# Performance work log

Measured on AMD Instinct MI355X. Metric: run time of the kernel, lower is better.

The kernel has to match this reference:

```python
import jax, jax.numpy as jnp
import numpy as np

B, F, H, W = 1, 6, 20, 26
S = F * H * W            # 3120 tokens
DIM, NH, HD = 1536, 12, 128
C = HD // 2              # 64 rotary channels
T_C = C - 2 * (C // 3)   # 22 temporal channels
H_C = C // 3             # 21
W_C = C // 3             # 21
LOCAL_FRAMES = 4         # local_attn_size (in frames)
SINK_FRAMES = 1          # sink_size (in frames)
EPS = 1e-6
MAX_POS = 1024


def _angle_table(n_ch):
    inv = 1.0 / (10000.0 ** (np.arange(n_ch, dtype=np.float64) / n_ch))
    return np.outer(np.arange(MAX_POS, dtype=np.float64), inv)


def setup_inputs() -> dict:
    key = jax.random.key(0)
    ks = jax.random.split(key, 8)
    sc = 0.02
    ang = np.concatenate([_angle_table(T_C), _angle_table(H_C), _angle_table(W_C)], axis=1)  # [1024, 64]
    return {
        "x": jax.random.normal(ks[0], (B, S, DIM), jnp.float32),
        "seq_lens": jnp.array([S], jnp.int32),
        "grid_sizes": jnp.array([[F, H, W]], jnp.int32),
        "freqs_cos": jnp.asarray(np.cos(ang), jnp.float32),
        "freqs_sin": jnp.asarray(np.sin(ang), jnp.float32),
        "Wq": jax.random.normal(ks[1], (DIM, DIM), jnp.float32) * sc,
        "bq": jnp.zeros((DIM,), jnp.float32),
        "Wk": jax.random.normal(ks[2], (DIM, DIM), jnp.float32) * sc,
        "bk": jnp.zeros((DIM,), jnp.float32),
        "Wv": jax.random.normal(ks[3], (DIM, DIM), jnp.float32) * sc,
        "bv": jnp.zeros((DIM,), jnp.float32),
        "Wo": jax.random.normal(ks[4], (DIM, DIM), jnp.float32) * sc,
        "bo": jnp.zeros((DIM,), jnp.float32),
        "gq": jnp.ones((DIM,), jnp.float32),
        "gk": jnp.ones((DIM,), jnp.float32),
    }


def _rms_norm(x, g):
    # WanRMSNorm: x * rsqrt(mean(x^2) + eps) * weight
    return x * jax.lax.rsqrt(jnp.mean(x * x, axis=-1, keepdims=True) + EPS) * g


def _rope_apply(x, freqs_cos, freqs_sin):
    # x: [B, S, NH, HD]; per-token 3D (f,h,w) rotary on consecutive pairs.
    pos = jnp.arange(S)
    f = pos // (H * W)
    hh = (pos // W) % H
    ww = pos % W
    cos_t, cos_h, cos_w = freqs_cos[:, :T_C], freqs_cos[:, T_C:T_C + H_C], freqs_cos[:, T_C + H_C:]
    sin_t, sin_h, sin_w = freqs_sin[:, :T_C], freqs_sin[:, T_C:T_C + H_C], freqs_sin[:, T_C + H_C:]
    cos = jnp.concatenate([cos_t[f], cos_h[hh], cos_w[ww]], axis=-1)[None, :, None, :]  # [1,S,1,C]
    sin = jnp.concatenate([sin_t[f], sin_h[hh], sin_w[ww]], axis=-1)[None, :, None, :]
    xp = x.reshape(B, S, NH, C, 2)
    xr, xi = xp[..., 0], xp[..., 1]
    out = jnp.stack([xr * cos - xi * sin, xr * sin + xi * cos], axis=-1)
    return out.reshape(B, S, NH, HD)


def _block_mask():
    # frame-causal + local window (in frames) + sink frames: [S, S] bool
    fid = jnp.arange(S) // (H * W)
    fi, fj = fid[:, None], fid[None, :]
    return (fj <= fi) & ((fi - fj < LOCAL_FRAMES) | (fj < SINK_FRAMES))


def reference(x, seq_lens, grid_sizes, freqs_cos, freqs_sin,
              Wq, bq, Wk, bk, Wv, bv, Wo, bo, gq, gk):
    q = _rms_norm(x @ Wq + bq, gq).reshape(B, S, NH, HD)
    k = _rms_norm(x @ Wk + bk, gk).reshape(B, S, NH, HD)
    v = (x @ Wv + bv).reshape(B, S, NH, HD)
    rq = _rope_apply(q, freqs_cos, freqs_sin)
    rk = _rope_apply(k, freqs_cos, freqs_sin)
    scale = 1.0 / jnp.sqrt(jnp.asarray(HD, x.dtype))
    scores = jnp.einsum('bind,bjnd->bnij', rq, rk) * scale  # [B,NH,S,S]
    scores = jnp.where(_block_mask()[None, None], scores, jnp.finfo(scores.dtype).min)
    attn = jax.nn.softmax(scores, axis=-1)
    out = jnp.einsum('bnij,bjnd->bind', attn, v).reshape(B, S, DIM)
    return out @ Wo + bo
```

## Files before the change

kernel.cpp:

```cpp
#include <hip/hip_runtime.h>
#include <hip/hip_bf16.h>
#include <stdint.h>

typedef short v8s __attribute__((ext_vector_type(8)));
typedef short v4h __attribute__((ext_vector_type(4)));
typedef float v4f __attribute__((ext_vector_type(4)));
typedef unsigned short u16;

#define S_LEN 3120
#define DIMN 1536
#define NHEAD 12
#define HDIM 128
#define FRM 520
#define NT64 49
#define T64_PH 166
#define TOT64 1992
#define NSTEP32 17
#define SCALE_QK 0.088388347648318447f
#define MAXOFF 12.0f

struct TaskMap {
  unsigned char tile[T64_PH];
  unsigned char frame[T64_PH];
  short accv[NT64];
  unsigned char nf[NT64];
};
constexpr TaskMap make_map() {
  TaskMap m{};
  int acc = 0;
  for (int tile = 0; tile < NT64; ++tile) {
    int q0t = tile * 64;
    int f_lo = q0t / FRM;
    int qhi = q0t + 63 < S_LEN - 1 ? q0t + 63 : S_LEN - 1;
    int f_hi = qhi / FRM;
    int fstart = f_lo - 3 > 0 ? f_lo - 3 : 0;
    int sink = fstart > 0 ? 1 : 0;
    int nf = f_hi - fstart + 1 + sink;
    m.accv[tile] = (short)acc;
    m.nf[tile] = (unsigned char)nf;
    for (int c = 0; c < nf; ++c) {
      m.tile[acc + c] = (unsigned char)tile;
      m.frame[acc + c] = (unsigned char)(sink ? (c == 0 ? 0 : fstart + c - 1) : (fstart + c));
    }
    acc += nf;
  }
  return m;
}
__device__ __constant__ TaskMap TM = make_map();

__device__ __forceinline__ v4f mfma16(v8s a, v8s b, v4f c) {
  return __builtin_amdgcn_mfma_f32_16x16x32_bf16(a, b, c, 0, 0, 0);
}
__device__ __forceinline__ float b2f(u16 u) {
  union { float f; unsigned int i; } x; x.i = ((unsigned int)u) << 16; return x.f;
}
__device__ __forceinline__ u16 f2b(float f) {
  union { float f; unsigned int i; } x; x.f = f;
  unsigned int r = x.i + 0x7FFFu + ((x.i >> 16) & 1u);
  return (u16)(r >> 16);
}
__device__ __forceinline__ void async16(const void* g, void* l) {
  __builtin_amdgcn_global_load_lds(
      (__attribute__((address_space(1))) const void*)g,
      (__attribute__((address_space(3))) void*)l, 16, 0, 0);
}

__global__ void detect_dtype(const u16* __restrict__ w, int* __restrict__ flag) {
  __shared__ int sh;
  int t = threadIdx.x;
  if (t == 0) sh = 0;
  __syncthreads();
  u16 m0 = (u16)(w[2 * t] & 0x7FFF);
  u16 m1 = (u16)(w[2 * t + 1] & 0x7FFF);
  if (m0 >= 0x4480 || m1 >= 0x4480) atomicOr(&sh, 1);
  __syncthreads();
  if (t == 0) *flag = sh;
}

struct PrepArgs {
  const void* tin[4]; u16* tout[4];
  const void* csrc[9]; u16* cdst[9]; int cn[9];
};
__global__ __launch_bounds__(256) void prep(PrepArgs a, const int* __restrict__ flag) {
  int isf = *flag;
  int z = blockIdx.z;
  int t = threadIdx.x;
  int bidx = blockIdx.y * gridDim.x + blockIdx.x;
  if (z < 4) {
    const float* inf = (const float*)a.tin[z];
    const u16* inb = (const u16*)a.tin[z];
    u16* out = a.tout[z];
    int row = (bidx % 24) * 64 + (t & 63);
    int c0 = (bidx / 24) * 16 + (t >> 6) * 4;
    float v[4];
    if (isf) {
      float4 d = *(const float4*)(inf + (size_t)row * DIMN + c0);
      v[0] = d.x; v[1] = d.y; v[2] = d.z; v[3] = d.w;
    } else {
      ushort4 d = *(const ushort4*)(inb + (size_t)row * DIMN + c0);
      v[0] = b2f(d.x); v[1] = b2f(d.y); v[2] = b2f(d.z); v[3] = b2f(d.w);
    }
#pragma unroll
    for (int k = 0; k < 4; ++k)
      out[(size_t)(c0 + k) * DIMN + row] = f2b(v[k]);
  } else {
    int id = z - 4;
    int n4 = a.cn[id] >> 2;
    const float* sf = (const float*)a.csrc[id];
    const u16* sb = (const u16*)a.csrc[id];
    u16* d = a.cdst[id];
    int stride = gridDim.x * gridDim.y * 256;
    for (int i = bidx * 256 + t; i < n4; i += stride) {
      v4h o;
      if (isf) {
        float4 x4 = *(const float4*)(sf + (size_t)i * 4);
        o[0] = (short)f2b(x4.x); o[1] = (short)f2b(x4.y);
        o[2] = (short)f2b(x4.z); o[3] = (short)f2b(x4.w);
      } else {
        o = *(const v4h*)(sb + (size_t)i * 4);
      }
      *(v4h*)(d + (size_t)i * 4) = o;
    }
  }
}

template <int MT, int NT>
__global__ __launch_bounds__(256) void gemm3(
    const u16* __restrict__ A,
    const u16* BT0, const u16* BT1, const u16* BT2,
    const u16* b0, const u16* b1, const u16* b2,
    void* C0, void* C1, void* C2, int M, const int* __restrict__ flag, int dyn) {
  static_assert(MT == 64, "4-wave layout assumes MT==64");
  const u16* BT; const u16* bias; void* C;
  if (blockIdx.z == 0)      { BT = BT0; bias = b0; C = C0; }
  else if (blockIdx.z == 1) { BT = BT1; bias = b1; C = C1; }
  else                      { BT = BT2; bias = b2; C = C2; }
  int f32out = dyn ? *flag : 0;
  __shared__ __align__(16) short As[MT * 64];
  __shared__ __align__(16) short Bs[NT * 64];
  int t = threadIdx.x, w = t >> 6, l = t & 63;
  int ln = l & 15, lg = l >> 4;
  int m0 = blockIdx.y * MT, n0 = blockIdx.x * NT;
  int lr = l >> 3;
  int gl = (l & 7) ^ lr;
  constexpr int ACH = MT / 32;
  constexpr int BCH = NT / 32;
  const u16* gAp[ACH]; short* lAp[ACH];
#pragma unroll
  for (int i = 0; i < ACH; ++i) {
    int c = w * ACH + i;
    int arow = min(m0 + c * 8 + lr, M - 1);
    gAp[i] = A + (size_t)arow * DIMN + gl * 8;
    lAp[i] = As + c * 512;
  }
  const u16* gBp[BCH]; short* lBp[BCH];
#pragma unroll
  for (int i = 0; i < BCH; ++i) {
    int c = w * BCH + i;
    int brow = n0 + c * 8 + lr;
    gBp[i] = BT + (size_t)brow * DIMN + gl * 8;
    lBp[i] = Bs + c * 512;
  }
  constexpr int NJ = NT / 64;
  int aoff[2][4], boff[2][NJ];
#pragma unroll
  for (int ks = 0; ks < 2; ++ks) {
#pragma unroll
    for (int i = 0; i < 4; ++i) {
      int ar = i * 16 + ln;
      aoff[ks][i] = ar * 64 + (((ks * 4 + lg) ^ (ar & 7)) * 8);
    }
#pragma unroll
    for (int j = 0; j < NJ; ++j) {
      int br = w * (NJ * 16) + j * 16 + ln;
      boff[ks][j] = br * 64 + (((ks * 4 + lg) ^ (br & 7)) * 8);
    }
  }
  v4f acc[4][NJ] = {};
  for (int k0 = 0; k0 < DIMN; k0 += 64) {
    __syncthreads();
#pragma unroll
    for (int i = 0; i < ACH; ++i) async16(gAp[i] + k0, lAp[i]);
#pragma unroll
    for (int i = 0; i < BCH; ++i) async16(gBp[i] + k0, lBp[i]);
    __syncthreads();
#pragma unroll
    for (int ks = 0; ks < 2; ++ks) {
      v8s af[4], bfr[NJ];
#pragma unroll
      for (int i = 0; i < 4; ++i) af[i] = *(const v8s*)(As + aoff[ks][i]);
#pragma unroll
      for (int j = 0; j < NJ; ++j) bfr[j] = *(const v8s*)(Bs + boff[ks][j]);
#pragma unroll
      for (int i = 0; i < 4; ++i)
#pragma unroll
        for (int j = 0; j < NJ; ++j) acc[i][j] = mfma16(af[i], bfr[j], acc[i][j]);
    }
  }
  if ((!dyn) && blockIdx.z == 2) {
#pragma unroll
    for (int i = 0; i < 4; ++i) {
      int rb = m0 + i * 16 + lg * 4;
      if (rb + 3 >= M) continue;
#pragma unroll
      for (int j = 0; j < NJ; ++j) {
        int col = n0 + w * (NJ * 16) + j * 16 + ln;
        float bv = b2f(bias[col]);
        v4h pk;
#pragma unroll
        for (int r = 0; r < 4; ++r) pk[r] = (short)f2b(acc[i][j][r] + bv);
        *(v4h*)((u16*)C + (size_t)col * S_LEN + rb) = pk;
      }
    }
    return;
  }
#pragma unroll
  for (int i = 0; i < 4; ++i) {
    int rb = m0 + i * 16 + lg * 4;
#pragma unroll
    for (int j = 0; j < NJ; ++j) {
      int col = n0 + w * (NJ * 16) + j * 16 + ln;
      float bv = b2f(bias[col]);
#pragma unroll
      for (int r = 0; r < 4; ++r) {
        int grow = rb + r;
        if (grow < M) {
          size_t idx = (size_t)grow * DIMN + col;
          float val = acc[i][j][r] + bv;
          if (f32out) ((float*)C)[idx] = val;
          else        ((u16*)C)[idx] = f2b(val);
        }
      }
    }
  }
}

__global__ __launch_bounds__(256) void norm_rope(u16* __restrict__ Q, u16* __restrict__ K,
                                                 const u16* __restrict__ gq,
                                                 const u16* __restrict__ gk,
                                                 const u16* __restrict__ fcos,
                                                 const u16* __restrict__ fsin) {
  int t = threadIdx.x, w = t >> 6, l = t & 63;
  int s = blockIdx.x * 4 + w;
  u16* base = (blockIdx.y == 0 ? Q : K) + (size_t)s * DIMN;
  const u16* g = (blockIdx.y == 0) ? gq : gk;
  v8s xv[3], gv[3];
#pragma unroll
  for (int c = 0; c < 3; ++c) {
    xv[c] = *(const v8s*)(base + c * 512 + l * 8);
    gv[c] = *(const v8s*)(g + c * 512 + l * 8);
  }
  float x[24];
  float ss = 0.f;
#pragma unroll
  for (int c = 0; c < 3; ++c)
#pragma unroll
    for (int j = 0; j < 8; ++j) {
      float v = b2f((u16)xv[c][j]);
      x[c * 8 + j] = v;
      ss += v * v;
    }
#pragma unroll
  for (int off = 32; off > 0; off >>= 1) ss += __shfl_xor(ss, off);
  float rs = rsqrtf(ss * (1.0f / DIMN) + 1e-6f);
  int f = s / FRM;
  int hh = (s / 26) % 20;
  int ww = s % 26;
#pragma unroll
  for (int c = 0; c < 3; ++c) {
    v8s out;
#pragma unroll
    for (int u = 0; u < 4; ++u) {
      int e0 = c * 512 + l * 8 + 2 * u;
      int ch = (e0 & 127) >> 1;
      int p = (ch < 22) ? f : ((ch < 43) ? hh : ww);
      float co = b2f(fcos[p * 64 + ch]);
      float si = b2f(fsin[p * 64 + ch]);
      float xr = x[c * 8 + 2 * u] * rs * b2f((u16)gv[c][2 * u]);
      float xi = x[c * 8 + 2 * u + 1] * rs * b2f((u16)gv[c][2 * u + 1]);
      out[2 * u]     = (short)f2b(xr * co - xi * si);
      out[2 * u + 1] = (short)f2b(xr * si + xi * co);
    }
    *(v8s*)(base + c * 512 + l * 8) = out;
  }
}

__global__ __launch_bounds__(128) void attn_block(const u16* __restrict__ Q,
                                                  const u16* __restrict__ K,
                                                  const u16* __restrict__ VT,
                                                  u16* __restrict__ Po,
                                                  float* __restrict__ Pl) {
  __shared__ __align__(16) short Ks[2][32 * 128];
  __shared__ __align__(16) short Vs[2][128 * 32];
  __shared__ __align__(16) short Pt[2][32 * 40];
  int t = threadIdx.x, w = t >> 6, l = t & 63;
  int ln = l & 15, lg = l >> 4;
  int task = blockIdx.x;
  int head = task / T64_PH, tid = task % T64_PH;
  int tile = TM.tile[tid], frame = TM.frame[tid];
  int q0 = tile * 64 + w * 32;
  v8s qf[2][4];
  bool rowok[2][4];
#pragma unroll
  for (int g = 0; g < 2; ++g) {
    int row = min(q0 + g * 16 + ln, S_LEN - 1);
    const u16* qp = Q + (size_t)row * DIMN + head * HDIM + lg * 8;
#pragma unroll
    for (int c = 0; c < 4; ++c) qf[g][c] = *(const v8s*)(qp + c * 32);
#pragma unroll
    for (int r = 0; r < 4; ++r) {
      int qr = q0 + g * 16 + lg * 4 + r;
      int fi = (qr < S_LEN) ? qr / FRM : -1;
      rowok[g][r] = (frame <= fi) && ((fi - frame) < 4 || frame == 0);
    }
  }
  float lsum[2][4] = {};
  v4f o[2][8] = {};
  int kbeg = frame * FRM, kend = kbeg + FRM;
  int kr_i[4], kgl_i[4], vd_i[4], vgl_i[4];
#pragma unroll
  for (int i = 0; i < 4; ++i) {
    int n = (w * 4 + i) * 64 + l;
    kr_i[i] = n >> 4;
    kgl_i[i] = (n & 15) ^ (kr_i[i] & 15);
    vd_i[i] = n >> 2;
    vgl_i[i] = (n & 3) ^ (vd_i[i] & 3);
  }
  const u16* Kb = K + head * HDIM;
  {
    int kb = kbeg;
#pragma unroll
    for (int i = 0; i < 4; ++i) {
      int krow = min(kb + kr_i[i], S_LEN - 1);
      async16(Kb + (size_t)krow * DIMN + kgl_i[i] * 8,
              (char*)Ks + (size_t)(w * 4 + i) * 1024);
      async16(VT + (size_t)(head * HDIM + vd_i[i]) * S_LEN + kb + vgl_i[i] * 8,
              (char*)Vs + (size_t)(w * 4 + i) * 1024);
    }
  }
  __syncthreads();
  for (int it = 0; it < NSTEP32; ++it) {
    int cur = it & 1;
    if (it + 1 < NSTEP32) {
      int kbn = kbeg + (it + 1) * 32;
      size_t boff = (size_t)(cur ^ 1) * 8192;
#pragma unroll
      for (int i = 0; i < 4; ++i) {
        int krow = min(kbn + kr_i[i], S_LEN - 1);
        async16(Kb + (size_t)krow * DIMN + kgl_i[i] * 8,
                (char*)Ks + boff + (size_t)(w * 4 + i) * 1024);
        async16(VT + (size_t)(head * HDIM + vd_i[i]) * S_LEN + kbn + vgl_i[i] * 8,
                (char*)Vs + boff + (size_t)(w * 4 + i) * 1024);
      }
    }
    int kb = kbeg + it * 32;
    v4f s[2][2] = {};
    __builtin_amdgcn_s_setprio(1);
#pragma unroll
    for (int kg = 0; kg < 2; ++kg) {
#pragma unroll
      for (int c = 0; c < 4; ++c) {
        v8s kf = *(const v8s*)(&Ks[cur][(kg * 16 + ln) * 128 + (((c * 4 + lg) ^ ln) * 8)]);
        s[0][kg] = mfma16(qf[0][c], kf, s[0][kg]);
        s[1][kg] = mfma16(qf[1][c], kf, s[1][kg]);
      }
    }
    __builtin_amdgcn_s_setprio(0);
#pragma unroll
    for (int g = 0; g < 2; ++g)
#pragma unroll
      for (int kg = 0; kg < 2; ++kg) {
        bool jv = (kb + kg * 16 + ln) < kend;
#pragma unroll
        for (int r = 0; r < 4; ++r) {
          float p = (rowok[g][r] && jv) ? __expf(s[g][kg][r] * SCALE_QK - MAXOFF) : 0.f;
          unsigned int bi = __float_as_uint(p) & 0xffff0000u;
          lsum[g][r] += __uint_as_float(bi);
          Pt[w][(g * 16 + lg * 4 + r) * 40 + kg * 16 + ln] = (u16)(bi >> 16);
        }
      }
    v8s pf0 = *(const v8s*)(&Pt[w][ln * 40 + lg * 8]);
    v8s pf1 = *(const v8s*)(&Pt[w][(16 + ln) * 40 + lg * 8]);
    __builtin_amdgcn_s_setprio(1);
#pragma unroll
    for (int d = 0; d < 8; ++d) {
      int rr = d * 16 + ln;
      v8s vf = *(const v8s*)(&Vs[cur][rr * 32 + ((lg ^ (rr & 3)) * 8)]);
      o[0][d] = mfma16(pf0, vf, o[0][d]);
      o[1][d] = mfma16(pf1, vf, o[1][d]);
    }
    __builtin_amdgcn_s_setprio(0);
    __syncthreads();
  }
#pragma unroll
  for (int g = 0; g < 2; ++g)
#pragma unroll
    for (int r = 0; r < 4; ++r) {
      float v = lsum[g][r];
      v += __shfl_xor(v, 1);
      v += __shfl_xor(v, 2);
      v += __shfl_xor(v, 4);
      v += __shfl_xor(v, 8);
      lsum[g][r] = v;
    }
  size_t pbase = (size_t)task * (64 * 128);
#pragma unroll
  for (int g = 0; g < 2; ++g)
#pragma unroll
    for (int d = 0; d < 8; ++d)
#pragma unroll
      for (int r = 0; r < 4; ++r) {
        int lrow = w * 32 + g * 16 + lg * 4 + r;
        Po[pbase + lrow * 128 + d * 16 + ln] = f2b(o[g][d][r]);
      }
  if (ln == 0) {
#pragma unroll
    for (int g = 0; g < 2; ++g)
#pragma unroll
      for (int r = 0; r < 4; ++r)
        Pl[task * 64 + w * 32 + g * 16 + lg * 4 + r] = lsum[g][r];
  }
}

__global__ __launch_bounds__(256) void attn_combine(const u16* __restrict__ Po,
                                                    const float* __restrict__ Pl,
                                                    u16* __restrict__ Oa) {
  int tile = blockIdx.x, h = blockIdx.y;
  int accv = TM.accv[tile], nf = TM.nf[tile];
  int base = h * T64_PH + accv;
  int t = threadIdx.x;
  int row = t >> 2, seg = (t & 3) * 32;
  int grow = tile * 64 + row;
  if (grow >= S_LEN) return;
  float lsum = 0.f;
  float ao[32];
#pragma unroll
  for (int j = 0; j < 32; ++j) ao[j] = 0.f;
  for (int c = 0; c < nf; ++c) {
    int task = base + c;
    lsum += Pl[task * 64 + row];
    const u16* p = Po + (size_t)task * 8192 + row * 128 + seg;
#pragma unroll
    for (int v = 0; v < 4; ++v) {
      v8s x = *(const v8s*)(p + v * 8);
#pragma unroll
      for (int j = 0; j < 8; ++j) ao[v * 8 + j] += b2f((u16)x[j]);
    }
  }
  float inv = 1.0f / lsum;
  u16* dst = Oa + (size_t)grow * DIMN + h * HDIM + seg;
#pragma unroll
  for (int v = 0; v < 4; ++v) {
    v8s res;
#pragma unroll
    for (int j = 0; j < 8; ++j) res[j] = (short)f2b(ao[v * 8 + j] * inv);
    *(v8s*)(dst + v * 8) = res;
  }
}

extern "C" void kernel_launch(void* const* d_in, const int* in_sizes, int n_in,
                              void* d_out, int out_size, void* d_ws, size_t ws_size,
                              hipStream_t stream) {
  (void)n_in; (void)out_size; (void)ws_size;
  int* flag = (int*)d_ws;
  u16* ws = (u16*)d_ws;
  size_t off = 16;
  const size_t SD = (size_t)S_LEN * DIMN;
  const size_t WW = (size_t)DIMN * DIMN;
  const size_t NPO = (size_t)1032 * 128 * 128;
  auto alloc = [&](size_t n) { u16* p = ws + off; off += (n + 7) & ~(size_t)7; return p; };
  u16* Xc  = alloc(SD);
  u16* Fc  = alloc(65536);
  u16* Fs  = alloc(65536);
  u16* bqc = alloc(1536); u16* bkc = alloc(1536); u16* bvc = alloc(1536); u16* boc = alloc(1536);
  u16* gqc = alloc(1536); u16* gkc = alloc(1536);
  u16* Qr = alloc(SD); u16* Kr = alloc(SD);
  u16* VT = alloc(SD);
  u16* Oa = alloc(SD);
  u16* WoT = alloc(WW);
  u16* WqT = alloc(WW); u16* WkT = alloc(WW); u16* WvT = alloc(WW);
  alloc(NPO - 3 * WW);
  float* Pl = (float*)alloc((size_t)TOT64 * 64 * 2);
  u16* Po = WqT;

  detect_dtype<<<1, 256, 0, stream>>>((const u16*)d_in[5], flag);

  PrepArgs pa;
  pa.tin[0] = d_in[5];  pa.tout[0] = WqT;
  pa.tin[1] = d_in[7];  pa.tout[1] = WkT;
  pa.tin[2] = d_in[9];  pa.tout[2] = WvT;
  pa.tin[3] = d_in[11]; pa.tout[3] = WoT;
  const int srcIdx[9] = {0, 3, 4, 6, 8, 10, 12, 13, 14};
  u16* dsts[9] = {Xc, Fc, Fs, bqc, bkc, bvc, boc, gqc, gkc};
  for (int i = 0; i < 9; ++i) {
    pa.csrc[i] = d_in[srcIdx[i]];
    pa.cdst[i] = dsts[i];
    pa.cn[i] = in_sizes[srcIdx[i]];
  }
  dim3 b256(256);
  prep<<<dim3(48, 48, 13), b256, 0, stream>>>(pa, flag);
  gemm3<64, 128><<<dim3(12, 49, 3), b256, 0, stream>>>(Xc, WqT, WkT, WvT, bqc, bkc, bvc,
                                                       Qr, Kr, VT, S_LEN, flag, 0);
  norm_rope<<<dim3(S_LEN / 4, 2), b256, 0, stream>>>(Qr, Kr, gqc, gkc, Fc, Fs);
  attn_block<<<dim3(TOT64), dim3(128), 0, stream>>>(Qr, Kr, VT, Po, Pl);
  attn_combine<<<dim3(NT64, NHEAD), b256, 0, stream>>>(Po, Pl, Oa);
  gemm3<64, 128><<<dim3(12, 49, 1), b256, 0, stream>>>(Oa, WoT, WoT, WoT, boc, boc, boc,
                                                       d_out, d_out, d_out, S_LEN, flag, 1);
}
```

Baseline: 349.3 us.

## Split attention tile across four waves and use shared-memory tiled weight transpose

The attention block kernel now runs 256 threads per block, with each of four waves owning 16 query rows instead of two waves owning 32. This halves per-wave register state and the per-wave share of K/V async loads, aiming for more latency hiding. Separately, the weight-transpose prep path now stages 32x32 tiles through padded shared memory so that both reads and writes are coalesced, replacing the strided scatter stores. The trade-off is more waves per block, each doing less MFMA work per K/V tile load, and an added barrier in prep.

```diff
diff --git a/kernel.cpp b/kernel.cpp
--- a/kernel.cpp
+++ b/kernel.cpp
@@ -87,22 +87,24 @@
   int t = threadIdx.x;
   int bidx = blockIdx.y * gridDim.x + blockIdx.x;
   if (z < 4) {
+    __shared__ u16 tile[32][33];
     const float* inf = (const float*)a.tin[z];
     const u16* inb = (const u16*)a.tin[z];
     u16* out = a.tout[z];
-    int row = (bidx % 24) * 64 + (t & 63);
-    int c0 = (bidx / 24) * 16 + (t >> 6) * 4;
-    float v[4];
-    if (isf) {
-      float4 d = *(const float4*)(inf + (size_t)row * DIMN + c0);
-      v[0] = d.x; v[1] = d.y; v[2] = d.z; v[3] = d.w;
-    } else {
-      ushort4 d = *(const ushort4*)(inb + (size_t)row * DIMN + c0);
-      v[0] = b2f(d.x); v[1] = b2f(d.y); v[2] = b2f(d.z); v[3] = b2f(d.w);
-    }
-#pragma unroll
-    for (int k = 0; k < 4; ++k)
-      out[(size_t)(c0 + k) * DIMN + row] = f2b(v[k]);
+    int tx = t & 31, ty = t >> 5;
+    int gr0 = blockIdx.y * 32, gc0 = blockIdx.x * 32;
+#pragma unroll
+    for (int i = 0; i < 4; ++i) {
+      int r = ty + i * 8;
+      size_t idx = (size_t)(gr0 + r) * DIMN + gc0 + tx;
+      tile[r][tx] = isf ? f2b(inf[idx]) : inb[idx];
+    }
+    __syncthreads();
+#pragma unroll
+    for (int i = 0; i < 4; ++i) {
+      int r = ty + i * 8;
+      out[(size_t)(gc0 + r) * DIMN + gr0 + tx] = tile[tx][r];
+    }
   } else {
     int id = z - 4;
     int n4 = a.cn[id] >> 2;
@@ -285,42 +287,41 @@
   }
 }
 
-__global__ __launch_bounds__(128) void attn_block(const u16* __restrict__ Q,
+__global__ __launch_bounds__(256) void attn_block(const u16* __restrict__ Q,
                                                   const u16* __restrict__ K,
                                                   const u16* __restrict__ VT,
                                                   u16* __restrict__ Po,
                                                   float* __restrict__ Pl) {
   __shared__ __align__(16) short Ks[2][32 * 128];
   __shared__ __align__(16) short Vs[2][128 * 32];
-  __shared__ __align__(16) short Pt[2][32 * 40];
+  __shared__ __align__(16) short Pt[4][16 * 40];
   int t = threadIdx.x, w = t >> 6, l = t & 63;
   int ln = l & 15, lg = l >> 4;
   int task = blockIdx.x;
   int head = task / T64_PH, tid = task % T64_PH;
   int tile = TM.tile[tid], frame = TM.frame[tid];
-  int q0 = tile * 64 + w * 32;
-  v8s qf[2][4];
-  bool rowok[2][4];
-#pragma unroll
-  for (int g = 0; g < 2; ++g) {
-    int row = min(q0 + g * 16 + ln, S_LEN - 1);
+  int q0 = tile * 64 + w * 16;
+  v8s qf[4];
+  bool rowok[4];
+  {
+    int row = min(q0 + ln, S_LEN - 1);
     const u16* qp = Q + (size_t)row * DIMN + head * HDIM + lg * 8;
 #pragma unroll
-    for (int c = 0; c < 4; ++c) qf[g][c] = *(const v8s*)(qp + c * 32);
+    for (int c = 0; c < 4; ++c) qf[c] = *(const v8s*)(qp + c * 32);
 #pragma unroll
     for (int r = 0; r < 4; ++r) {
-      int qr = q0 + g * 16 + lg * 4 + r;
+      int qr = q0 + lg * 4 + r;
       int fi = (qr < S_LEN) ? qr / FRM : -1;
-      rowok[g][r] = (frame <= fi) && ((fi - frame) < 4 || frame == 0);
-    }
-  }
-  float lsum[2][4] = {};
-  v4f o[2][8] = {};
+      rowok[r] = (frame <= fi) && ((fi - frame) < 4 || frame == 0);
+    }
+  }
+  float lsum[4] = {};
+  v4f o[8] = {};
   int kbeg = frame * FRM, kend = kbeg + FRM;
-  int kr_i[4], kgl_i[4], vd_i[4], vgl_i[4];
-#pragma unroll
-  for (int i = 0; i < 4; ++i) {
-    int n = (w * 4 + i) * 64 + l;
+  int kr_i[2], kgl_i[2], vd_i[2], vgl_i[2];
+#pragma unroll
+  for (int i = 0; i < 2; ++i) {
+    int n = (w * 2 + i) * 64 + l;
     kr_i[i] = n >> 4;
     kgl_i[i] = (n & 15) ^ (kr_i[i] & 15);
     vd_i[i] = n >> 2;
@@ -330,12 +331,12 @@
   {
     int kb = kbeg;
 #pragma unroll
-    for (int i = 0; i < 4; ++i) {
+    for (int i = 0; i < 2; ++i) {
       int krow = min(kb + kr_i[i], S_LEN - 1);
       async16(Kb + (size_t)krow * DIMN + kgl_i[i] * 8,
-              (char*)Ks + (size_t)(w * 4 + i) * 1024);
+              (char*)Ks + (size_t)(w * 2 + i) * 1024);
       async16(VT + (size_t)(head * HDIM + vd_i[i]) * S_LEN + kb + vgl_i[i] * 8,
-              (char*)Vs + (size_t)(w * 4 + i) * 1024);
+              (char*)Vs + (size_t)(w * 2 + i) * 1024);
     }
   }
   __syncthreads();
@@ -345,80 +346,69 @@
       int kbn = kbeg + (it + 1) * 32;
       size_t boff = (size_t)(cur ^ 1) * 8192;
 #pragma unroll
-      for (int i = 0; i < 4; ++i) {
+      for (int i = 0; i < 2; ++i) {
         int krow = min(kbn + kr_i[i], S_LEN - 1);
         async16(Kb + (size_t)krow * DIMN + kgl_i[i] * 8,
-                (char*)Ks + boff + (size_t)(w * 4 + i) * 1024);
+                (char*)Ks + boff + (size_t)(w * 2 + i) * 1024);
         async16(VT + (size_t)(head * HDIM + vd_i[i]) * S_LEN + kbn + vgl_i[i] * 8,
-                (char*)Vs + boff + (size_t)(w * 4 + i) * 1024);
+                (char*)Vs + boff + (size_t)(w * 2 + i) * 1024);
       }
     }
     int kb = kbeg + it * 32;
-    v4f s[2][2] = {};
+    v4f s[2] = {};
     __builtin_amdgcn_s_setprio(1);
 #pragma unroll
     for (int kg = 0; kg < 2; ++kg) {
 #pragma unroll
       for (int c = 0; c < 4; ++c) {
         v8s kf = *(const v8s*)(&Ks[cur][(kg * 16 + ln) * 128 + (((c * 4 + lg) ^ ln) * 8)]);
-        s[0][kg] = mfma16(qf[0][c], kf, s[0][kg]);
-        s[1][kg] = mfma16(qf[1][c], kf, s[1][kg]);
+        s[kg] = mfma16(qf[c], kf, s[kg]);
       }
     }
     __builtin_amdgcn_s_setprio(0);
 #pragma unroll
-    for (int g = 0; g < 2; ++g)
-#pragma unroll
-      for (int kg = 0; kg < 2; ++kg) {
-        bool jv = (kb + kg * 16 + ln) < kend;
-#pragma unroll
-        for (int r = 0; r < 4; ++r) {
-          float p = (rowok[g][r] && jv) ? __expf(s[g][kg][r] * SCALE_QK - MAXOFF) : 0.f;
-          unsigned int bi = __float_as_uint(p) & 0xffff0000u;
-          lsum[g][r] += __uint_as_float(bi);
-          Pt[w][(g * 16 + lg * 4 + r) * 40 + kg * 16 + ln] = (u16)(bi >> 16);
-        }
-      }
+    for (int kg = 0; kg < 2; ++kg) {
+      bool jv = (kb + kg * 16 + ln) < kend;
+#pragma unroll
+      for (int r = 0; r < 4; ++r) {
+        float p = (rowok[r] && jv) ? __expf(s[kg][r] * SCALE_QK - MAXOFF) : 0.f;
+        unsigned int bi = __float_as_uint(p) & 0xffff0000u;
+        lsum[r] += __uint_as_float(bi);
+        Pt[w][(lg * 4 + r) * 40 + kg * 16 + ln] = (u16)(bi >> 16);
+      }
+    }
     v8s pf0 = *(const v8s*)(&Pt[w][ln * 40 + lg * 8]);
-    v8s pf1 = *(const v8s*)(&Pt[w][(16 + ln) * 40 + lg * 8]);
     __builtin_amdgcn_s_setprio(1);
 #pragma unroll
     for (int d = 0; d < 8; ++d) {
       int rr = d * 16 + ln;
       v8s vf = *(const v8s*)(&Vs[cur][rr * 32 + ((lg ^ (rr & 3)) * 8)]);
-      o[0][d] = mfma16(pf0, vf, o[0][d]);
-      o[1][d] = mfma16(pf1, vf, o[1][d]);
+      o[d] = mfma16(pf0, vf, o[d]);
     }
     __builtin_amdgcn_s_setprio(0);
     __syncthreads();
   }
 #pragma unroll
-  for (int g = 0; g < 2; ++g)
+  for (int r = 0; r < 4; ++r) {
+    float v = lsum[r];
+    v += __shfl_xor(v, 1);
+    v += __shfl_xor(v, 2);
+    v += __shfl_xor(v, 4);
+    v += __shfl_xor(v, 8);
+    lsum[r] = v;
+  }
+  size_t pbase = (size_t)task * (64 * 128);
+#pragma unroll
+  for (int d = 0; d < 8; ++d)
 #pragma unroll
     for (int r = 0; r < 4; ++r) {
-      float v = lsum[g][r];
-      v += __shfl_xor(v, 1);
-      v += __shfl_xor(v, 2);
-      v += __shfl_xor(v, 4);
-      v += __shfl_xor(v, 8);
-      lsum[g][r] = v;
-    }
-  size_t pbase = (size_t)task * (64 * 128);
-#pragma unroll
-  for (int g = 0; g < 2; ++g)
-#pragma unroll
-    for (int d = 0; d < 8; ++d)
-#pragma unroll
-      for (int r = 0; r < 4; ++r) {
-        int lrow = w * 32 + g * 16 + lg * 4 + r;
-        Po[pbase + lrow * 128 + d * 16 + ln] = f2b(o[g][d][r]);
-      }
+      int lrow = w * 16 + lg * 4 + r;
+      Po[pbase + lrow * 128 + d * 16 + ln] = f2b(o[d][r]);
+    }
   if (ln == 0) {
 #pragma unroll
-    for (int g = 0; g < 2; ++g)
-#pragma unroll
-      for (int r = 0; r < 4; ++r)
-        Pl[task * 64 + w * 32 + g * 16 + lg * 4 + r] = lsum[g][r];
+    for (int r = 0; r < 4; ++r)
+      Pl[task * 64 + w * 16 + lg * 4 + r] = lsum[r];
   }
 }
 
@@ -502,7 +492,7 @@
   gemm3<64, 128><<<dim3(12, 49, 3), b256, 0, stream>>>(Xc, WqT, WkT, WvT, bqc, bkc, bvc,
                                                        Qr, Kr, VT, S_LEN, flag, 0);
   norm_rope<<<dim3(S_LEN / 4, 2), b256, 0, stream>>>(Qr, Kr, gqc, gkc, Fc, Fs);
-  attn_block<<<dim3(TOT64), dim3(128), 0, stream>>>(Qr, Kr, VT, Po, Pl);
+  attn_block<<<dim3(TOT64), dim3(256), 0, stream>>>(Qr, Kr, VT, Po, Pl);
   attn_combine<<<dim3(NT64, NHEAD), b256, 0, stream>>>(Po, Pl, Oa);
   gemm3<64, 128><<<dim3(12, 49, 1), b256, 0, stream>>>(Oa, WoT, WoT, WoT, boc, boc, boc,
                                                        d_out, d_out, d_out, S_LEN, flag, 1);
```

Result: no change. 344.1 us (-1.5%).
